# Kernel tuning notes

Measured on AMD Instinct MI355X. Metric: run time of the kernel, lower is better.

The kernel has to match this reference:

```python
import jax, jax.numpy as jnp
import numpy as np

N_HEAD = 16
NEG_BIG = 1e10

def setup_inputs() -> dict:
    key = jax.random.key(0)
    k1, k2, k3 = jax.random.split(key, 3)
    B, S, D = 2, 2048, 1024
    x = jax.random.normal(k1, (B, S, D), dtype=jnp.float32)
    c_attn_w = jax.random.normal(k2, (D, 3 * D), dtype=jnp.float32) * 0.02
    c_attn_b = jnp.zeros((3 * D,), dtype=jnp.float32)
    c_proj_w = jax.random.normal(k3, (D, D), dtype=jnp.float32) * 0.02
    c_proj_b = jnp.zeros((D,), dtype=jnp.float32)
    return {"x": x, "c_attn_w": c_attn_w, "c_attn_b": c_attn_b,
            "c_proj_w": c_proj_w, "c_proj_b": c_proj_b}

def reference(x, c_attn_w, c_attn_b, c_proj_w, c_proj_b):
    B, S, D = x.shape
    H = N_HEAD
    hd = D // H
    # Conv1D c_attn: x @ W + b -> (B, S, 3D)
    qkv = x @ c_attn_w + c_attn_b
    q, k, v = jnp.split(qkv, 3, axis=-1)
    # split heads -> (B, H, S, hd)
    q = q.reshape(B, S, H, hd).transpose(0, 2, 1, 3)
    k = k.reshape(B, S, H, hd).transpose(0, 2, 1, 3)
    v = v.reshape(B, S, H, hd).transpose(0, 2, 1, 3)
    # QK^T with scale (scale=True)
    w = jnp.einsum('bhqd,bhkd->bhqk', q, k) / jnp.sqrt(jnp.float32(hd))
    # additive/multiplicative causal mask, exactly as source: w*b - 1e10*(1-b)
    b = jnp.tril(jnp.ones((S, S), dtype=w.dtype))
    w = w * b - NEG_BIG * (1.0 - b)
    w = jax.nn.softmax(w, axis=-1)
    a = jnp.einsum('bhqk,bhkd->bhqd', w, v)
    # merge heads -> (B, S, D)
    a = a.transpose(0, 2, 1, 3).reshape(B, S, D)
    # Conv1D c_proj
    a = a @ c_proj_w + c_proj_b
    # present = stack(key (as (B,H,S,hd)), value)
    present = jnp.stack((k, v))
    return (a, present)
```

## Files before the change

### kernel.cpp

```cpp
#include <hip/hip_runtime.h>
#include <hip/hip_bf16.h>
#include <string.h>

#define BB 2
#define SS 2048
#define DD 1024
#define NH 16
#define TT (BB * SS)
#define N3 (3 * DD)
#define A_SIZE (TT * DD)
#define PRESENT_HALF (BB * NH * SS * 64)
#define C2Q 0.18033688011112043f

typedef __attribute__((ext_vector_type(8))) short short8;
typedef __attribute__((ext_vector_type(4))) float floatx4;
typedef __attribute__((ext_vector_type(8))) unsigned short ushort8;

__device__ __forceinline__ unsigned short f2bf(float f) {
    union { float f; unsigned u; } v; v.f = f;
    unsigned r = v.u + 0x7fffu + ((v.u >> 16) & 1u);
    return (unsigned short)(r >> 16);
}
__device__ __forceinline__ unsigned pack2bf(float a, float b) {
    __hip_bfloat162 h = __float22bfloat162_rn(float2{a, b});
    unsigned u; memcpy(&u, &h, 4); return u;
}
__device__ __forceinline__ float bf2f(unsigned short u) {
    union { unsigned u; float f; } v; v.u = ((unsigned)u) << 16; return v.f;
}

__device__ __forceinline__ void async16(const unsigned short* g, unsigned short* lds) {
    __builtin_amdgcn_global_load_lds(
        (const __attribute__((address_space(1))) unsigned int*)g,
        (__attribute__((address_space(3))) unsigned int*)lds,
        16, 0, 0);
}

__global__ __launch_bounds__(256) void cast_x_kernel(const float* __restrict__ src,
                                                     unsigned short* __restrict__ dst) {
    int i = (blockIdx.x * 256 + threadIdx.x) * 8;
    float4 a = *(const float4*)(src + i);
    float4 b = *(const float4*)(src + i + 4);
    ushort8 o;
    o[0] = f2bf(a.x); o[1] = f2bf(a.y); o[2] = f2bf(a.z); o[3] = f2bf(a.w);
    o[4] = f2bf(b.x); o[5] = f2bf(b.y); o[6] = f2bf(b.z); o[7] = f2bf(b.w);
    *(ushort8*)(dst + i) = o;
}

__global__ __launch_bounds__(256) void transpose_cast_kernel(const float* __restrict__ src,
                                                             unsigned short* __restrict__ dst,
                                                             int R, int C) {
    __shared__ float tile[32][33];
    int c0 = blockIdx.x * 32, r0 = blockIdx.y * 32;
    int tx = threadIdx.x, ty = threadIdx.y;
    for (int i = ty; i < 32; i += 8)
        tile[i][tx] = src[(size_t)(r0 + i) * C + c0 + tx];
    __syncthreads();
    for (int i = ty; i < 32; i += 8)
        dst[(size_t)(c0 + i) * R + r0 + tx] = f2bf(tile[tx][i]);
}

__global__ __launch_bounds__(256)
void vtrans_kernel(const unsigned short* __restrict__ qkv,
                   unsigned short* __restrict__ vT) {
    __shared__ unsigned short tile[64][72];
    int bh = blockIdx.x, st = blockIdx.y;
    int b = bh >> 4, h = bh & 15;
    int tid = threadIdx.x;
    int r = tid >> 2, c = (tid & 3) * 16;
    const unsigned short* src = qkv + ((size_t)(b * SS + st * 64 + r)) * 3072 + 2048 + h * 64 + c;
    *(int4*)(&tile[r][c])     = *(const int4*)(src);
    *(int4*)(&tile[r][c + 8]) = *(const int4*)(src + 8);
    __syncthreads();
    int d = tid >> 2, s0 = (tid & 3) * 16;
    unsigned short tmp[16];
    for (int e = 0; e < 16; ++e) tmp[e] = tile[s0 + e][d];
    unsigned short* dst = vT + ((size_t)bh * 64 + d) * SS + st * 64 + s0;
    *(int4*)(dst)     = *(const int4*)(tmp);
    *(int4*)(dst + 8) = *(const int4*)(tmp + 8);
}

__global__ __launch_bounds__(256)
void present_kernel(const unsigned short* __restrict__ qkvb, float* __restrict__ out) {
    size_t e = ((size_t)blockIdx.x * 256 + threadIdx.x) * 8;
    int d = (int)(e & 63);
    int s = (int)((e >> 6) & 2047);
    int h = (int)((e >> 17) & 15);
    int b = (int)((e >> 21) & 1);
    int half = (int)(e >> 22);
    const unsigned short* src = qkvb + ((size_t)(b * SS + s)) * 3072 + 1024 + half * 1024 + h * 64 + d;
    ushort8 u = *(const ushort8*)src;
    float* dst = out + A_SIZE + e;
    float4 f0 = {bf2f(u[0]), bf2f(u[1]), bf2f(u[2]), bf2f(u[3])};
    float4 f1 = {bf2f(u[4]), bf2f(u[5]), bf2f(u[6]), bf2f(u[7])};
    *(float4*)(dst) = f0;
    *(float4*)(dst + 4) = f1;
}

__global__ __launch_bounds__(256)
void gemm_kernel(const unsigned short* __restrict__ A,
                 const unsigned short* __restrict__ Bt,
                 const float* __restrict__ bias,
                 int mode,
                 unsigned short* __restrict__ out_bf,
                 float* __restrict__ out_f) {
    __shared__ unsigned short As[2][128][32];
    __shared__ unsigned short Bs[2][128][32];
    const int tid  = threadIdx.x;
    const int t0   = blockIdx.y * 128;
    const int n0   = blockIdx.x * 128;
    const int wave = tid >> 6, lane = tid & 63;
    const int wm = wave >> 1, wn = wave & 1;
    const int l15 = lane & 15, quad = lane >> 4;

    const int sr = lane >> 2;
    const int sc = (lane & 3) * 8;

    floatx4 acc[4][4];
    for (int i = 0; i < 4; ++i)
        for (int j = 0; j < 4; ++j)
            for (int e = 0; e < 4; ++e) acc[i][j][e] = 0.f;

    const unsigned short* gA = A  + (size_t)(t0 + wave * 32 + sr) * 1024 + sc;
    const unsigned short* gB = Bt + (size_t)(n0 + wave * 32 + sr) * 1024 + sc;

    async16(gA,             &As[0][wave * 32][0]);
    async16(gA + 16 * 1024, &As[0][wave * 32 + 16][0]);
    async16(gB,             &Bs[0][wave * 32][0]);
    async16(gB + 16 * 1024, &Bs[0][wave * 32 + 16][0]);

    for (int kt = 0; kt < 32; ++kt) {
        const int cur = kt & 1;
        __syncthreads();
        if (kt < 31) {
            const int k1 = (kt + 1) * 32;
            async16(gA + k1,             &As[cur ^ 1][wave * 32][0]);
            async16(gA + k1 + 16 * 1024, &As[cur ^ 1][wave * 32 + 16][0]);
            async16(gB + k1,             &Bs[cur ^ 1][wave * 32][0]);
            async16(gB + k1 + 16 * 1024, &Bs[cur ^ 1][wave * 32 + 16][0]);
        }
        short8 af[4], bfr[4];
        for (int mt = 0; mt < 4; ++mt)
            af[mt] = *(const short8*)(&As[cur][wm * 64 + mt * 16 + l15][quad * 8]);
        for (int nt = 0; nt < 4; ++nt)
            bfr[nt] = *(const short8*)(&Bs[cur][wn * 64 + nt * 16 + l15][quad * 8]);
        for (int mt = 0; mt < 4; ++mt)
            for (int nt = 0; nt < 4; ++nt)
                acc[mt][nt] = __builtin_amdgcn_mfma_f32_16x16x32_bf16(bfr[nt], af[mt], acc[mt][nt], 0, 0, 0);
    }

    const float qs = (mode == 0 && n0 < 1024) ? C2Q : 1.0f;
    for (int mt = 0; mt < 4; ++mt) {
        const int t = t0 + wm * 64 + mt * 16 + l15;
        if (mode == 0) {
            unsigned short* po = out_bf + (size_t)t * 3072 + n0 + wn * 64;
            for (int nt = 0; nt < 4; ++nt) {
                float4 b4 = *(const float4*)(bias + n0 + wn * 64 + nt * 16 + quad * 4);
                float v0 = (acc[mt][nt][0] + b4.x) * qs;
                float v1 = (acc[mt][nt][1] + b4.y) * qs;
                float v2 = (acc[mt][nt][2] + b4.z) * qs;
                float v3 = (acc[mt][nt][3] + b4.w) * qs;
                uint2 w = {pack2bf(v0, v1), pack2bf(v2, v3)};
                *(uint2*)(po + nt * 16 + quad * 4) = w;
            }
        } else {
            float* po = out_f + (size_t)t * 1024 + n0 + wn * 64;
            for (int nt = 0; nt < 4; ++nt) {
                float4 b4 = *(const float4*)(bias + n0 + wn * 64 + nt * 16 + quad * 4);
                float4 v = {acc[mt][nt][0] + b4.x, acc[mt][nt][1] + b4.y,
                            acc[mt][nt][2] + b4.z, acc[mt][nt][3] + b4.w};
                *(float4*)(po + nt * 16 + quad * 4) = v;
            }
        }
    }
}

__global__ __launch_bounds__(256)
void flash_kernel(const unsigned short* __restrict__ qkv,
                  const unsigned short* __restrict__ vT,
                  unsigned short* __restrict__ out) {
    __shared__ unsigned short Kt[2][64][72];
    __shared__ unsigned short Vt[2][64][72];
    __shared__ unsigned short Pt[4][16][72];

    const int bh = blockIdx.x;
    const int qt = 31 - blockIdx.y;
    const int b = bh >> 4, h = bh & 15;
    const int tid = threadIdx.x;
    const int wave = tid >> 6, lane = tid & 63;
    const int l15 = lane & 15, quad = lane >> 4;

    const size_t rowb = (size_t)b * SS;
    const int kcol = 1024 + h * 64;

    short8 bq0, bq1;
    {
        const unsigned short* qp = qkv + (rowb + qt * 64 + wave * 16 + l15) * 3072 + h * 64 + quad * 8;
        bq0 = *(const short8*)(qp);
        bq1 = *(const short8*)(qp + 32);
    }

    float l_i = 0.f;
    floatx4 o[4];
    for (int dt = 0; dt < 4; ++dt)
        for (int e = 0; e < 4; ++e) o[dt][e] = 0.f;

    const int qrow_l = wave * 16 + l15;

    const int rr = tid >> 3, seg = (tid & 7) * 8;
    const int vr = tid >> 2, vc = (tid & 3) * 16;
    const unsigned short* kb = qkv + rowb * 3072 + kcol;
    const unsigned short* vb = vT + (size_t)bh * 64 * SS;
    int4 ka0, ka1, va0, va1;

    #define PREF(j) { \
        const unsigned short* ks = kb + (size_t)((j) * 64 + rr) * 3072 + seg; \
        ka0 = *(const int4*)(ks); \
        ka1 = *(const int4*)(ks + 32 * 3072); \
        const unsigned short* vs = vb + (size_t)vr * SS + (j) * 64 + vc; \
        va0 = *(const int4*)(vs); \
        va1 = *(const int4*)(vs + 8); }
    #define STAGE(bf_) { \
        *(int4*)(&Kt[bf_][rr][seg])      = ka0; \
        *(int4*)(&Kt[bf_][rr + 32][seg]) = ka1; \
        *(int4*)(&Vt[bf_][vr][vc])       = va0; \
        *(int4*)(&Vt[bf_][vr][vc + 8])   = va1; }

    PREF(0);
    STAGE(0);
    if (qt > 0) PREF(1);

    for (int j = 0; j <= qt; ++j) {
        const int cur = j & 1;
        __syncthreads();
        if (j < qt) {
            STAGE(cur ^ 1);
            if (j + 2 <= qt) PREF(j + 2);
        }

        floatx4 sc[4];
        for (int nt = 0; nt < 4; ++nt)
            for (int e = 0; e < 4; ++e) sc[nt][e] = 0.f;
        for (int nt = 0; nt < 4; ++nt) {
            const unsigned short* kp = &Kt[cur][nt * 16 + l15][quad * 8];
            short8 ak0 = *(const short8*)(kp);
            short8 ak1 = *(const short8*)(kp + 32);
            sc[nt] = __builtin_amdgcn_mfma_f32_16x16x32_bf16(ak0, bq0, sc[nt], 0, 0, 0);
            sc[nt] = __builtin_amdgcn_mfma_f32_16x16x32_bf16(ak1, bq1, sc[nt], 0, 0, 0);
        }
        if (j == qt) {
            for (int nt = 0; nt < 4; ++nt)
                for (int r = 0; r < 4; ++r)
                    if (nt * 16 + quad * 4 + r > qrow_l) sc[nt][r] = -1.0e30f;
        }

        for (int nt = 0; nt < 4; ++nt)
            for (int r = 0; r < 4; ++r) {
                float p = __builtin_amdgcn_exp2f(sc[nt][r]);
                sc[nt][r] = p;
                l_i += p;
            }

        for (int nt = 0; nt < 4; ++nt) {
            uint2 w = {pack2bf(sc[nt][0], sc[nt][1]), pack2bf(sc[nt][2], sc[nt][3])};
            *(uint2*)(&Pt[wave][l15][nt * 16 + quad * 4]) = w;
        }
        asm volatile("s_waitcnt lgkmcnt(0)" ::: "memory");
        short8 bp0 = *(const short8*)(&Pt[wave][l15][quad * 8]);
        short8 bp1 = *(const short8*)(&Pt[wave][l15][32 + quad * 8]);
        for (int dt = 0; dt < 4; ++dt) {
            const unsigned short* vp = &Vt[cur][dt * 16 + l15][quad * 8];
            short8 av0 = *(const short8*)(vp);
            short8 av1 = *(const short8*)(vp + 32);
            o[dt] = __builtin_amdgcn_mfma_f32_16x16x32_bf16(av0, bp0, o[dt], 0, 0, 0);
            o[dt] = __builtin_amdgcn_mfma_f32_16x16x32_bf16(av1, bp1, o[dt], 0, 0, 0);
        }
    }
    #undef PREF
    #undef STAGE

    l_i += __shfl_xor(l_i, 16);
    l_i += __shfl_xor(l_i, 32);
    float inv = 1.f / l_i;
    const int qrow = qt * 64 + wave * 16 + l15;
    unsigned short* po = out + (rowb + qrow) * 1024 + h * 64;
    for (int dt = 0; dt < 4; ++dt) {
        uint2 w = {pack2bf(o[dt][0] * inv, o[dt][1] * inv),
                   pack2bf(o[dt][2] * inv, o[dt][3] * inv)};
        *(uint2*)(po + dt * 16 + quad * 4) = w;
    }
}

extern "C" void kernel_launch(void* const* d_in, const int* in_sizes, int n_in,
                              void* d_out, int out_size, void* d_ws, size_t ws_size,
                              hipStream_t stream) {
    const float* x        = (const float*)d_in[0];
    const float* c_attn_w = (const float*)d_in[1];
    const float* c_attn_b = (const float*)d_in[2];
    const float* c_proj_w = (const float*)d_in[3];
    const float* c_proj_b = (const float*)d_in[4];
    float* out = (float*)d_out;

    char* ws = (char*)d_ws;
    unsigned short* xb     = (unsigned short*)(ws);
    unsigned short* wqkvt  = (unsigned short*)(ws + 8388608);
    unsigned short* wprojt = (unsigned short*)(ws + 14680064);
    unsigned short* qkvb   = (unsigned short*)(ws + 16777216);
    unsigned short* aout   = (unsigned short*)(ws + 41943040);
    unsigned short* vT     = xb;

    cast_x_kernel<<<(TT * DD) / (256 * 8), 256, 0, stream>>>(x, xb);
    transpose_cast_kernel<<<dim3(N3 / 32, DD / 32), dim3(32, 8), 0, stream>>>(c_attn_w, wqkvt, DD, N3);
    transpose_cast_kernel<<<dim3(DD / 32, DD / 32), dim3(32, 8), 0, stream>>>(c_proj_w, wprojt, DD, DD);
    gemm_kernel<<<dim3(N3 / 128, TT / 128), 256, 0, stream>>>(xb, wqkvt, c_attn_b, 0, qkvb, out);
    present_kernel<<<(2 * PRESENT_HALF) / (256 * 8), 256, 0, stream>>>(qkvb, out);
    vtrans_kernel<<<dim3(32, 32), 256, 0, stream>>>(qkvb, vT);
    flash_kernel<<<dim3(32, 32), 256, 0, stream>>>(qkvb, vT, aout);
    gemm_kernel<<<dim3(DD / 128, TT / 128), 256, 0, stream>>>(aout, wprojt, c_proj_b, 1, nullptr, out);
}
```

Baseline: 215.5 us.

## Add dedicated 256x256-tile QKV GEMM with triple-buffered async loads

Replaces the generic 128x128 GEMM for the QKV projection with a specialised kernel. It uses 512 threads, 256x256 output tiles, a three-stage async LDS pipeline with explicit waitcnt/barrier control, and MFMA priority hints. The larger tiles raise data reuse per block and the pipeline overlaps global loads with compute. The cost is that only 192 blocks are launched, fewer than the CU count, which may underfill the device.

```diff
diff --git a/kernel.cpp b/kernel.cpp
--- a/kernel.cpp
+++ b/kernel.cpp
@@ -11,6 +11,7 @@
 #define A_SIZE (TT * DD)
 #define PRESENT_HALF (BB * NH * SS * 64)
 #define C2Q 0.18033688011112043f
+#define NTK 32
 
 typedef __attribute__((ext_vector_type(8))) short short8;
 typedef __attribute__((ext_vector_type(4))) float floatx4;
@@ -95,6 +96,110 @@
     float4 f1 = {bf2f(u[4]), bf2f(u[5]), bf2f(u[6]), bf2f(u[7])};
     *(float4*)(dst) = f0;
     *(float4*)(dst + 4) = f1;
+}
+
+__global__ __launch_bounds__(512, 2)
+void gemm_qkv_kernel(const unsigned short* __restrict__ A,
+                     const unsigned short* __restrict__ Bt,
+                     const float* __restrict__ bias,
+                     unsigned short* __restrict__ out_bf) {
+    __shared__ unsigned short As3[3][16][512];
+    __shared__ unsigned short Bs3[3][16][512];
+    const int tid  = threadIdx.x;
+    const int wave = tid >> 6, lane = tid & 63;
+    const int l15 = lane & 15, quad = lane >> 4;
+    const int wm = wave >> 2, wn = wave & 3;
+    const int t0 = blockIdx.y * 256;
+    const int n0 = blockIdx.x * 256;
+
+    floatx4 acc[8][4];
+    #pragma unroll
+    for (int i = 0; i < 8; ++i)
+        #pragma unroll
+        for (int j = 0; j < 4; ++j)
+            #pragma unroll
+            for (int e = 0; e < 4; ++e) acc[i][j][e] = 0.f;
+
+    const unsigned short* gA = A  + (size_t)(t0 + wave * 32 + l15) * 1024 + quad * 8;
+    const unsigned short* gB = Bt + (size_t)(n0 + wave * 32 + l15) * 1024 + quad * 8;
+
+    async16(gA,                 &As3[0][2 * wave][0]);
+    async16(gA + 16 * 1024,     &As3[0][2 * wave + 1][0]);
+    async16(gB,                 &Bs3[0][2 * wave][0]);
+    async16(gB + 16 * 1024,     &Bs3[0][2 * wave + 1][0]);
+    async16(gA + 32,            &As3[1][2 * wave][0]);
+    async16(gA + 32 + 16 * 1024,&As3[1][2 * wave + 1][0]);
+    async16(gB + 32,            &Bs3[1][2 * wave][0]);
+    async16(gB + 32 + 16 * 1024,&Bs3[1][2 * wave + 1][0]);
+
+    const unsigned short* gA2 = gA + 64;
+    const unsigned short* gB2 = gB + 64;
+
+    int bc = 0;
+    for (int t = 0; t < NTK; ++t) {
+        const int bp = (bc >= 1) ? bc - 1 : 2;
+
+        asm volatile("s_waitcnt lgkmcnt(0)" ::: "memory");
+        if (t == NTK - 1) { asm volatile("s_waitcnt vmcnt(0)" ::: "memory"); }
+        else              { asm volatile("s_waitcnt vmcnt(4)" ::: "memory"); }
+        asm volatile("" ::: "memory");
+        __builtin_amdgcn_s_barrier();
+        asm volatile("" ::: "memory");
+
+        const unsigned short* aB = &As3[bc][wm * 8][0] + lane * 8;
+        const unsigned short* bB = &Bs3[bc][wn * 4][0] + lane * 8;
+
+        if (t < NTK - 2) {
+            async16(gA2,             &As3[bp][2 * wave][0]);
+            async16(gA2 + 16 * 1024, &As3[bp][2 * wave + 1][0]);
+        }
+        short8 af[8], bf[4];
+        #pragma unroll
+        for (int mt = 0; mt < 4; ++mt) af[mt] = *(const short8*)(aB + mt * 512);
+        #pragma unroll
+        for (int nt = 0; nt < 4; ++nt) bf[nt] = *(const short8*)(bB + nt * 512);
+        __builtin_amdgcn_s_setprio(1);
+        #pragma unroll
+        for (int mt = 0; mt < 4; ++mt)
+            #pragma unroll
+            for (int nt = 0; nt < 4; ++nt)
+                acc[mt][nt] = __builtin_amdgcn_mfma_f32_16x16x32_bf16(bf[nt], af[mt], acc[mt][nt], 0, 0, 0);
+        __builtin_amdgcn_s_setprio(0);
+
+        if (t < NTK - 2) {
+            async16(gB2,             &Bs3[bp][2 * wave][0]);
+            async16(gB2 + 16 * 1024, &Bs3[bp][2 * wave + 1][0]);
+            gA2 += 32; gB2 += 32;
+        }
+        #pragma unroll
+        for (int mt = 4; mt < 8; ++mt) af[mt] = *(const short8*)(aB + mt * 512);
+        __builtin_amdgcn_s_setprio(1);
+        #pragma unroll
+        for (int mt = 4; mt < 8; ++mt)
+            #pragma unroll
+            for (int nt = 0; nt < 4; ++nt)
+                acc[mt][nt] = __builtin_amdgcn_mfma_f32_16x16x32_bf16(bf[nt], af[mt], acc[mt][nt], 0, 0, 0);
+        __builtin_amdgcn_s_setprio(0);
+
+        bc = (bc == 2) ? 0 : bc + 1;
+    }
+
+    const float qs = (n0 < 1024) ? C2Q : 1.0f;
+    #pragma unroll
+    for (int mt = 0; mt < 8; ++mt) {
+        const int t = t0 + wm * 128 + mt * 16 + l15;
+        unsigned short* po = out_bf + (size_t)t * 3072 + n0 + wn * 64;
+        #pragma unroll
+        for (int nt = 0; nt < 4; ++nt) {
+            float4 b4 = *(const float4*)(bias + n0 + wn * 64 + nt * 16 + quad * 4);
+            float v0 = (acc[mt][nt][0] + b4.x) * qs;
+            float v1 = (acc[mt][nt][1] + b4.y) * qs;
+            float v2 = (acc[mt][nt][2] + b4.z) * qs;
+            float v3 = (acc[mt][nt][3] + b4.w) * qs;
+            uint2 w = {pack2bf(v0, v1), pack2bf(v2, v3)};
+            *(uint2*)(po + nt * 16 + quad * 4) = w;
+        }
+    }
 }
 
 __global__ __launch_bounds__(256)
@@ -312,7 +417,7 @@
     cast_x_kernel<<<(TT * DD) / (256 * 8), 256, 0, stream>>>(x, xb);
     transpose_cast_kernel<<<dim3(N3 / 32, DD / 32), dim3(32, 8), 0, stream>>>(c_attn_w, wqkvt, DD, N3);
     transpose_cast_kernel<<<dim3(DD / 32, DD / 32), dim3(32, 8), 0, stream>>>(c_proj_w, wprojt, DD, DD);
-    gemm_kernel<<<dim3(N3 / 128, TT / 128), 256, 0, stream>>>(xb, wqkvt, c_attn_b, 0, qkvb, out);
+    gemm_qkv_kernel<<<dim3(N3 / 256, TT / 256), 512, 0, stream>>>(xb, wqkvt, c_attn_b, qkvb);
     present_kernel<<<(2 * PRESENT_HALF) / (256 * 8), 256, 0, stream>>>(qkvb, out);
     vtrans_kernel<<<dim3(32, 32), 256, 0, stream>>>(qkvb, vT);
     flash_kernel<<<dim3(32, 32), 256, 0, stream>>>(qkvb, vT, aout);
```

New measurement: 229.0 us. 6.3% more time.

## Add dedicated 256x192 QKV GEMM kernel with phased async prefetch pipeline

Applied to the files above, without the earlier changes.

Replaces the generic 128x128 GEMM used for the QKV projection with a new 512-thread kernel. Each block computes a 256x192 tile using MFMA 16x16x32 bf16 instructions, with double-buffered LDS fed by async global-to-LDS loads that are spread across four MFMA phases per k-step, plus setprio around the MFMA blocks. The aim is more reuse per loaded tile and better overlap of loads with MFMA work in the largest GEMM. In exchange the kernel uses many barriers and a tightly hand-tuned vmcnt wait schedule, which makes it fragile, and the grid is coarser (16x16 blocks).

```diff
diff --git a/kernel.cpp b/kernel.cpp
--- a/kernel.cpp
+++ b/kernel.cpp
@@ -11,6 +11,7 @@
 #define A_SIZE (TT * DD)
 #define PRESENT_HALF (BB * NH * SS * 64)
 #define C2Q 0.18033688011112043f
+#define NKT 16
 
 typedef __attribute__((ext_vector_type(8))) short short8;
 typedef __attribute__((ext_vector_type(4))) float floatx4;
@@ -95,6 +96,159 @@
     float4 f1 = {bf2f(u[4]), bf2f(u[5]), bf2f(u[6]), bf2f(u[7])};
     *(float4*)(dst) = f0;
     *(float4*)(dst + 4) = f1;
+}
+
+__global__ __launch_bounds__(512, 2)
+void gemm_qkv_kernel(const unsigned short* __restrict__ A,
+                     const unsigned short* __restrict__ Bt,
+                     const float* __restrict__ bias,
+                     unsigned short* __restrict__ out_bf) {
+    __shared__ unsigned short As2[2][32][512];
+    __shared__ unsigned short Bs2[2][24][512];
+    const int tid = threadIdx.x;
+    const int wave = tid >> 6, lane = tid & 63;
+    const int l15 = lane & 15, quad = lane >> 4;
+    const int wm = wave >> 2, wn = wave & 3;
+    const int t0 = blockIdx.y * 256;
+    const int n0 = blockIdx.x * 192;
+
+    floatx4 acc[8][3];
+    #pragma unroll
+    for (int i = 0; i < 8; ++i)
+        #pragma unroll
+        for (int j = 0; j < 3; ++j)
+            #pragma unroll
+            for (int e = 0; e < 4; ++e) acc[i][j][e] = 0.f;
+
+    const int afh = (wave < 4) ? wave : wave + 4;
+    const int ash = afh + 4;
+    const int bx  = 8 + (wave >> 1), bks = wave & 1;
+    const unsigned short* gA_fh = A  + (size_t)(t0 + afh * 16 + l15) * 1024 + quad * 8;
+    const unsigned short* gA_sh = A  + (size_t)(t0 + ash * 16 + l15) * 1024 + quad * 8;
+    const unsigned short* gB_a  = Bt + (size_t)(n0 + wave * 16 + l15) * 1024 + quad * 8;
+    const unsigned short* gB_b  = Bt + (size_t)(n0 + bx * 16 + l15) * 1024 + bks * 32 + quad * 8;
+
+    async16(gB_a,            &Bs2[0][wave * 2][0]);
+    async16(gB_a + 32,       &Bs2[0][wave * 2 + 1][0]);
+    async16(gB_b,            &Bs2[0][bx * 2 + bks][0]);
+    async16(gA_fh,           &As2[0][afh * 2][0]);
+    async16(gA_fh + 32,      &As2[0][afh * 2 + 1][0]);
+    async16(gA_sh,           &As2[0][ash * 2][0]);
+    async16(gA_sh + 32,      &As2[0][ash * 2 + 1][0]);
+    async16(gB_a + 64,       &Bs2[1][wave * 2][0]);
+    async16(gB_a + 96,       &Bs2[1][wave * 2 + 1][0]);
+    async16(gB_b + 64,       &Bs2[1][bx * 2 + bks][0]);
+    async16(gA_fh + 64,      &As2[1][afh * 2][0]);
+    async16(gA_fh + 96,      &As2[1][afh * 2 + 1][0]);
+    asm volatile("s_waitcnt vmcnt(5)" ::: "memory");
+    __builtin_amdgcn_s_barrier();
+    asm volatile("" ::: "memory");
+
+    #define MFMA_PH(mb)                                                                     \
+        __builtin_amdgcn_s_setprio(1);                                                      \
+        _Pragma("unroll")                                                                   \
+        for (int mi = 0; mi < 2; ++mi)                                                      \
+            _Pragma("unroll")                                                               \
+            for (int nt = 0; nt < 3; ++nt) {                                                \
+                acc[(mb) + mi][nt] = __builtin_amdgcn_mfma_f32_16x16x32_bf16(               \
+                    bfr[nt][0], af[mi][0], acc[(mb) + mi][nt], 0, 0, 0);                    \
+                acc[(mb) + mi][nt] = __builtin_amdgcn_mfma_f32_16x16x32_bf16(               \
+                    bfr[nt][1], af[mi][1], acc[(mb) + mi][nt], 0, 0, 0);                    \
+            }                                                                               \
+        __builtin_amdgcn_s_setprio(0);
+    #define BAR()                                                                           \
+        asm volatile("" ::: "memory");                                                      \
+        __builtin_amdgcn_s_barrier();                                                       \
+        asm volatile("" ::: "memory");
+
+    for (int t = 0; t < NKT; ++t) {
+        const int c = t & 1;
+        const unsigned short* aBase = &As2[c][wm * 16][0] + lane * 8;
+        const unsigned short* bBase = &Bs2[c][wn * 6][0] + lane * 8;
+        short8 bfr[3][2], af[2][2];
+
+        #pragma unroll
+        for (int nt = 0; nt < 3; ++nt)
+            #pragma unroll
+            for (int ks = 0; ks < 2; ++ks)
+                bfr[nt][ks] = *(const short8*)(bBase + (nt * 2 + ks) * 512);
+        af[0][0] = *(const short8*)(aBase);
+        af[0][1] = *(const short8*)(aBase + 512);
+        af[1][0] = *(const short8*)(aBase + 2 * 512);
+        af[1][1] = *(const short8*)(aBase + 3 * 512);
+        if (t < NKT - 1) {
+            const int k1 = (t + 1) * 64;
+            async16(gA_sh + k1,      &As2[c ^ 1][ash * 2][0]);
+            async16(gA_sh + k1 + 32, &As2[c ^ 1][ash * 2 + 1][0]);
+        }
+        BAR();
+        MFMA_PH(0);
+        asm volatile("s_waitcnt lgkmcnt(0)" ::: "memory");
+        BAR();
+
+        af[0][0] = *(const short8*)(aBase + 4 * 512);
+        af[0][1] = *(const short8*)(aBase + 5 * 512);
+        af[1][0] = *(const short8*)(aBase + 6 * 512);
+        af[1][1] = *(const short8*)(aBase + 7 * 512);
+        if (t < NKT - 2) {
+            const int k2 = (t + 2) * 64;
+            async16(gB_a + k2,      &Bs2[c][wave * 2][0]);
+            async16(gB_a + k2 + 32, &Bs2[c][wave * 2 + 1][0]);
+        }
+        BAR();
+        MFMA_PH(2);
+        asm volatile("s_waitcnt lgkmcnt(0)" ::: "memory");
+        BAR();
+
+        af[0][0] = *(const short8*)(aBase + 8 * 512);
+        af[0][1] = *(const short8*)(aBase + 9 * 512);
+        af[1][0] = *(const short8*)(aBase + 10 * 512);
+        af[1][1] = *(const short8*)(aBase + 11 * 512);
+        if (t < NKT - 2) {
+            const int k2 = (t + 2) * 64;
+            async16(gB_b + k2,  &Bs2[c][bx * 2 + bks][0]);
+            async16(gA_fh + k2, &As2[c][afh * 2][0]);
+        }
+        BAR();
+        MFMA_PH(4);
+        asm volatile("s_waitcnt lgkmcnt(0)" ::: "memory");
+        BAR();
+
+        af[0][0] = *(const short8*)(aBase + 12 * 512);
+        af[0][1] = *(const short8*)(aBase + 13 * 512);
+        af[1][0] = *(const short8*)(aBase + 14 * 512);
+        af[1][1] = *(const short8*)(aBase + 15 * 512);
+        if (t < NKT - 2) {
+            const int k2 = (t + 2) * 64;
+            async16(gA_fh + k2 + 32, &As2[c][afh * 2 + 1][0]);
+        }
+        BAR();
+        MFMA_PH(6);
+        asm volatile("s_waitcnt lgkmcnt(0)" ::: "memory");
+        if (t < NKT - 2)       { asm volatile("s_waitcnt vmcnt(5)" ::: "memory"); }
+        else if (t == NKT - 2) { asm volatile("s_waitcnt vmcnt(0)" ::: "memory"); }
+        BAR();
+    }
+    #undef MFMA_PH
+    #undef BAR
+
+    #pragma unroll
+    for (int mt = 0; mt < 8; ++mt) {
+        const int t = t0 + wm * 128 + mt * 16 + l15;
+        unsigned short* po = out_bf + (size_t)t * 3072 + n0 + wn * 48;
+        #pragma unroll
+        for (int nt = 0; nt < 3; ++nt) {
+            const int ncol = n0 + wn * 48 + nt * 16;
+            const float qs = (ncol < 1024) ? C2Q : 1.0f;
+            float4 b4 = *(const float4*)(bias + ncol + quad * 4);
+            float v0 = (acc[mt][nt][0] + b4.x) * qs;
+            float v1 = (acc[mt][nt][1] + b4.y) * qs;
+            float v2 = (acc[mt][nt][2] + b4.z) * qs;
+            float v3 = (acc[mt][nt][3] + b4.w) * qs;
+            uint2 w = {pack2bf(v0, v1), pack2bf(v2, v3)};
+            *(uint2*)(po + nt * 16 + quad * 4) = w;
+        }
+    }
 }
 
 __global__ __launch_bounds__(256)
@@ -312,7 +466,7 @@
     cast_x_kernel<<<(TT * DD) / (256 * 8), 256, 0, stream>>>(x, xb);
     transpose_cast_kernel<<<dim3(N3 / 32, DD / 32), dim3(32, 8), 0, stream>>>(c_attn_w, wqkvt, DD, N3);
     transpose_cast_kernel<<<dim3(DD / 32, DD / 32), dim3(32, 8), 0, stream>>>(c_proj_w, wprojt, DD, DD);
-    gemm_kernel<<<dim3(N3 / 128, TT / 128), 256, 0, stream>>>(xb, wqkvt, c_attn_b, 0, qkvb, out);
+    gemm_qkv_kernel<<<dim3(N3 / 192, TT / 256), 512, 0, stream>>>(xb, wqkvt, c_attn_b, qkvb);
     present_kernel<<<(2 * PRESENT_HALF) / (256 * 8), 256, 0, stream>>>(qkvb, out);
     vtrans_kernel<<<dim3(32, 32), 256, 0, stream>>>(qkvb, vT);
     flash_kernel<<<dim3(32, 32), 256, 0, stream>>>(qkvb, vT, aout);
```

After: 228.5 us. 6.1% more time.

## Fuse prep kernels, write present from QKV GEMM epilogue, prioritize MFMA waves

Applied to the files above, without the earlier changes.

Merges the x cast and both weight transpose-casts into a single prep kernel launch. The QKV GEMM epilogue now writes the K/V present tensor in fp32 directly, which removes the separate present kernel that re-read the bf16 QKV buffer. Flash attention raises wave priority around its MFMA blocks so matrix work is issued ahead of other waves. Present values are now written from fp32 before bf16 rounding, so precision changes slightly, and the GEMM epilogue does extra strided fp32 stores.

```diff
diff --git a/kernel.cpp b/kernel.cpp
--- a/kernel.cpp
+++ b/kernel.cpp
@@ -36,28 +36,41 @@
         16, 0, 0);
 }
 
-__global__ __launch_bounds__(256) void cast_x_kernel(const float* __restrict__ src,
-                                                     unsigned short* __restrict__ dst) {
-    int i = (blockIdx.x * 256 + threadIdx.x) * 8;
-    float4 a = *(const float4*)(src + i);
-    float4 b = *(const float4*)(src + i + 4);
-    ushort8 o;
-    o[0] = f2bf(a.x); o[1] = f2bf(a.y); o[2] = f2bf(a.z); o[3] = f2bf(a.w);
-    o[4] = f2bf(b.x); o[5] = f2bf(b.y); o[6] = f2bf(b.z); o[7] = f2bf(b.w);
-    *(ushort8*)(dst + i) = o;
-}
-
-__global__ __launch_bounds__(256) void transpose_cast_kernel(const float* __restrict__ src,
-                                                             unsigned short* __restrict__ dst,
-                                                             int R, int C) {
-    __shared__ float tile[32][33];
-    int c0 = blockIdx.x * 32, r0 = blockIdx.y * 32;
-    int tx = threadIdx.x, ty = threadIdx.y;
+__device__ __forceinline__ void tc_body(const float* __restrict__ src,
+                                        unsigned short* __restrict__ dst,
+                                        int R, int C, int bx, int by, int tid,
+                                        float (*tile)[33]) {
+    const int c0 = bx * 32, r0 = by * 32;
+    const int tx = tid & 31, ty = tid >> 5;
     for (int i = ty; i < 32; i += 8)
         tile[i][tx] = src[(size_t)(r0 + i) * C + c0 + tx];
     __syncthreads();
     for (int i = ty; i < 32; i += 8)
         dst[(size_t)(c0 + i) * R + r0 + tx] = f2bf(tile[tx][i]);
+}
+
+__global__ __launch_bounds__(256)
+void prep_kernel(const float* __restrict__ x, unsigned short* __restrict__ xb,
+                 const float* __restrict__ wqkv, unsigned short* __restrict__ wqkvt,
+                 const float* __restrict__ wproj, unsigned short* __restrict__ wprojt) {
+    __shared__ float tile[32][33];
+    const int bid = blockIdx.x;
+    const int tid = threadIdx.x;
+    if (bid < 2048) {
+        int i = (bid * 256 + tid) * 8;
+        float4 a = *(const float4*)(x + i);
+        float4 b = *(const float4*)(x + i + 4);
+        ushort8 o;
+        o[0] = f2bf(a.x); o[1] = f2bf(a.y); o[2] = f2bf(a.z); o[3] = f2bf(a.w);
+        o[4] = f2bf(b.x); o[5] = f2bf(b.y); o[6] = f2bf(b.z); o[7] = f2bf(b.w);
+        *(ushort8*)(xb + i) = o;
+    } else if (bid < 5120) {
+        const int bb = bid - 2048;
+        tc_body(wqkv, wqkvt, DD, N3, bb % 96, bb / 96, tid, tile);
+    } else {
+        const int bb = bid - 5120;
+        tc_body(wproj, wprojt, DD, DD, bb & 31, bb >> 5, tid, tile);
+    }
 }
 
 __global__ __launch_bounds__(256)
@@ -81,23 +94,6 @@
 }
 
 __global__ __launch_bounds__(256)
-void present_kernel(const unsigned short* __restrict__ qkvb, float* __restrict__ out) {
-    size_t e = ((size_t)blockIdx.x * 256 + threadIdx.x) * 8;
-    int d = (int)(e & 63);
-    int s = (int)((e >> 6) & 2047);
-    int h = (int)((e >> 17) & 15);
-    int b = (int)((e >> 21) & 1);
-    int half = (int)(e >> 22);
-    const unsigned short* src = qkvb + ((size_t)(b * SS + s)) * 3072 + 1024 + half * 1024 + h * 64 + d;
-    ushort8 u = *(const ushort8*)src;
-    float* dst = out + A_SIZE + e;
-    float4 f0 = {bf2f(u[0]), bf2f(u[1]), bf2f(u[2]), bf2f(u[3])};
-    float4 f1 = {bf2f(u[4]), bf2f(u[5]), bf2f(u[6]), bf2f(u[7])};
-    *(float4*)(dst) = f0;
-    *(float4*)(dst + 4) = f1;
-}
-
-__global__ __launch_bounds__(256)
 void gemm_kernel(const unsigned short* __restrict__ A,
                  const unsigned short* __restrict__ Bt,
                  const float* __restrict__ bias,
@@ -150,23 +146,36 @@
     }
 
     const float qs = (mode == 0 && n0 < 1024) ? C2Q : 1.0f;
+    const int cb = n0 + wn * 64;
     for (int mt = 0; mt < 4; ++mt) {
         const int t = t0 + wm * 64 + mt * 16 + l15;
         if (mode == 0) {
-            unsigned short* po = out_bf + (size_t)t * 3072 + n0 + wn * 64;
+            unsigned short* po = out_bf + (size_t)t * 3072 + cb;
+            float* pres = nullptr;
+            if (cb >= 1024) {
+                const int half = (cb >= 2048) ? 1 : 0;
+                const int h = (cb - 1024 - half * 1024) >> 6;
+                const int b = t >> 11, s = t & 2047;
+                pres = out_f + A_SIZE
+                     + (((size_t)(half * 2 + b)) * 16 + h) * (SS * 64) + (size_t)s * 64;
+            }
             for (int nt = 0; nt < 4; ++nt) {
-                float4 b4 = *(const float4*)(bias + n0 + wn * 64 + nt * 16 + quad * 4);
+                float4 b4 = *(const float4*)(bias + cb + nt * 16 + quad * 4);
                 float v0 = (acc[mt][nt][0] + b4.x) * qs;
                 float v1 = (acc[mt][nt][1] + b4.y) * qs;
                 float v2 = (acc[mt][nt][2] + b4.z) * qs;
                 float v3 = (acc[mt][nt][3] + b4.w) * qs;
                 uint2 w = {pack2bf(v0, v1), pack2bf(v2, v3)};
                 *(uint2*)(po + nt * 16 + quad * 4) = w;
+                if (pres) {
+                    float4 pv = {v0, v1, v2, v3};
+                    *(float4*)(pres + nt * 16 + quad * 4) = pv;
+                }
             }
         } else {
-            float* po = out_f + (size_t)t * 1024 + n0 + wn * 64;
+            float* po = out_f + (size_t)t * 1024 + cb;
             for (int nt = 0; nt < 4; ++nt) {
-                float4 b4 = *(const float4*)(bias + n0 + wn * 64 + nt * 16 + quad * 4);
+                float4 b4 = *(const float4*)(bias + cb + nt * 16 + quad * 4);
                 float4 v = {acc[mt][nt][0] + b4.x, acc[mt][nt][1] + b4.y,
                             acc[mt][nt][2] + b4.z, acc[mt][nt][3] + b4.w};
                 *(float4*)(po + nt * 16 + quad * 4) = v;
@@ -241,6 +250,7 @@
         floatx4 sc[4];
         for (int nt = 0; nt < 4; ++nt)
             for (int e = 0; e < 4; ++e) sc[nt][e] = 0.f;
+        __builtin_amdgcn_s_setprio(1);
         for (int nt = 0; nt < 4; ++nt) {
             const unsigned short* kp = &Kt[cur][nt * 16 + l15][quad * 8];
             short8 ak0 = *(const short8*)(kp);
@@ -248,6 +258,7 @@
             sc[nt] = __builtin_amdgcn_mfma_f32_16x16x32_bf16(ak0, bq0, sc[nt], 0, 0, 0);
             sc[nt] = __builtin_amdgcn_mfma_f32_16x16x32_bf16(ak1, bq1, sc[nt], 0, 0, 0);
         }
+        __builtin_amdgcn_s_setprio(0);
         if (j == qt) {
             for (int nt = 0; nt < 4; ++nt)
                 for (int r = 0; r < 4; ++r)
@@ -268,6 +279,7 @@
         asm volatile("s_waitcnt lgkmcnt(0)" ::: "memory");
         short8 bp0 = *(const short8*)(&Pt[wave][l15][quad * 8]);
         short8 bp1 = *(const short8*)(&Pt[wave][l15][32 + quad * 8]);
+        __builtin_amdgcn_s_setprio(1);
         for (int dt = 0; dt < 4; ++dt) {
             const unsigned short* vp = &Vt[cur][dt * 16 + l15][quad * 8];
             short8 av0 = *(const short8*)(vp);
@@ -275,6 +287,7 @@
             o[dt] = __builtin_amdgcn_mfma_f32_16x16x32_bf16(av0, bp0, o[dt], 0, 0, 0);
             o[dt] = __builtin_amdgcn_mfma_f32_16x16x32_bf16(av1, bp1, o[dt], 0, 0, 0);
         }
+        __builtin_amdgcn_s_setprio(0);
     }
     #undef PREF
     #undef STAGE
@@ -309,11 +322,8 @@
     unsigned short* aout   = (unsigned short*)(ws + 41943040);
     unsigned short* vT     = xb;
 
-    cast_x_kernel<<<(TT * DD) / (256 * 8), 256, 0, stream>>>(x, xb);
-    transpose_cast_kernel<<<dim3(N3 / 32, DD / 32), dim3(32, 8), 0, stream>>>(c_attn_w, wqkvt, DD, N3);
-    transpose_cast_kernel<<<dim3(DD / 32, DD / 32), dim3(32, 8), 0, stream>>>(c_proj_w, wprojt, DD, DD);
+    prep_kernel<<<6144, 256, 0, stream>>>(x, xb, c_attn_w, wqkvt, c_proj_w, wprojt);
     gemm_kernel<<<dim3(N3 / 128, TT / 128), 256, 0, stream>>>(xb, wqkvt, c_attn_b, 0, qkvb, out);
-    present_kernel<<<(2 * PRESENT_HALF) / (256 * 8), 256, 0, stream>>>(qkvb, out);
     vtrans_kernel<<<dim3(32, 32), 256, 0, stream>>>(qkvb, vT);
     flash_kernel<<<dim3(32, 32), 256, 0, stream>>>(qkvb, vT, aout);
     gemm_kernel<<<dim3(DD / 128, TT / 128), 256, 0, stream>>>(aout, wprojt, c_proj_b, 1, nullptr, out);
```

Measured after the change: 213.7 us. Within noise of the previous version (-0.8%).
